# Performance work log

Measured on AMD Instinct MI355X. Metric: run time of the kernel, lower is better.

The kernel has to match this reference:

```python
import jax, jax.numpy as jnp
import numpy as np

B, Nv, Ne, Dv, De, Du = 8, 4096, 32768, 128, 128, 128
Dep, Dvp, Dup = 128, 128, 128


def setup_inputs() -> dict:
    key = jax.random.key(0)
    ks = jax.random.split(key, 11)
    s = 0.02
    return {
        "nodes": jax.random.normal(ks[0], (B, Nv, Dv), jnp.float32),
        "edges": jax.random.normal(ks[1], (B, Ne, De), jnp.float32),
        "global_u": jax.random.normal(ks[2], (B, Du), jnp.float32),
        "edge_rs": jax.random.randint(ks[3], (B, Ne, 2), 0, Nv, jnp.int32),
        "edge_masks": jax.random.randint(ks[4], (B, Ne, 1), 0, 2, jnp.int32),
        "W_edge": jax.random.normal(ks[5], (De + 2 * Dv + Du, Dep), jnp.float32) * s,
        "b_edge": jnp.zeros((Dep,), jnp.float32),
        "W_node": jax.random.normal(ks[6], (Dep + Dv + Du, Dvp), jnp.float32) * s,
        "b_node": jnp.zeros((Dvp,), jnp.float32),
        "W_glob": jax.random.normal(ks[7], (Dep + Dvp + Du, Dup), jnp.float32) * s,
        "b_glob": jnp.zeros((Dup,), jnp.float32),
    }


def reference(nodes, edges, global_u, edge_rs, edge_masks,
              W_edge, b_edge, W_node, b_node, W_glob, b_glob):
    recv = edge_rs[..., 0]  # (B,Ne)
    send = edge_rs[..., 1]
    # gather receiver / sender node features: (B,Ne,Dv)
    r_nodes = jnp.take_along_axis(nodes, jnp.broadcast_to(recv[..., None], (B, Ne, Dv)), axis=1)
    s_nodes = jnp.take_along_axis(nodes, jnp.broadcast_to(send[..., None], (B, Ne, Dv)), axis=1)
    u_e = jnp.broadcast_to(global_u[:, None, :], (B, Ne, Du))

    # edge block: MLP on concat -> (B,Ne,Dep)
    edge_in = jnp.concatenate([edges, r_nodes, s_nodes, u_e], -1)
    edges_p = jax.nn.relu(edge_in @ W_edge + b_edge)

    # e2v merge: masked segment-sum of edges onto receiver nodes -> (B,Nv,Dep)
    mask = edge_masks.astype(edges_p.dtype)  # (B,Ne,1)
    e2v = jax.vmap(lambda e, r: jax.ops.segment_sum(e, r, num_segments=Nv))(edges_p * mask, recv)

    # node block
    u_n = jnp.broadcast_to(global_u[:, None, :], (B, Nv, Du))
    node_in = jnp.concatenate([e2v, nodes, u_n], -1)
    nodes_p = jax.nn.relu(node_in @ W_node + b_node)

    # global block: sum-pool edges and nodes
    e2u = edges_p.sum(axis=1)  # (B,Dep)
    v2u = nodes_p.sum(axis=1)  # (B,Dvp)
    global_in = jnp.concatenate([e2u, v2u, global_u], -1)
    global_u_p = jax.nn.relu(global_in @ W_glob + b_glob)

    return (nodes_p, edges_p, global_u_p)
```

## Files before the change

kernel.cpp:

```cpp
#include <hip/hip_runtime.h>
#include <hip/hip_bf16.h>

#define B  8
#define NV 4096
#define NE 32768
#define D  128
#define KE2 384
#define KN2 256
#define KG 384

using short8 = __attribute__((ext_vector_type(8))) short;
using f32x4  = __attribute__((ext_vector_type(4))) float;

__device__ inline unsigned short f2bf(float f) {
    unsigned u = __builtin_bit_cast(unsigned, f);
    u += 0x7FFFu + ((u >> 16) & 1u);
    return (unsigned short)(u >> 16);
}

__device__ inline short8 cvt8(float4 a, float4 b) {
    union { __hip_bfloat162 h[4]; short8 v; } u;
    u.h[0] = __float22bfloat162_rn(make_float2(a.x, a.y));
    u.h[1] = __float22bfloat162_rn(make_float2(a.z, a.w));
    u.h[2] = __float22bfloat162_rn(make_float2(b.x, b.y));
    u.h[3] = __float22bfloat162_rn(make_float2(b.z, b.w));
    return u.v;
}

__global__ __launch_bounds__(256) void prep_weights(
    const float* __restrict__ We, const float* __restrict__ Wn,
    unsigned short* __restrict__ WtE, unsigned short* __restrict__ WtN)
{
    const int idx = blockIdx.x * 256 + threadIdx.x;
    {
        const int n = idx / KE2, k = idx % KE2;
        WtE[idx] = f2bf(We[(size_t)k * D + n]);
    }
    if (idx < 128 * KN2) {
        const int n = idx >> 8, k = idx & 255;
        WtN[idx] = f2bf(Wn[(size_t)k * D + n]);
    }
}

__global__ __launch_bounds__(128) void bias_kernel(
    const float* __restrict__ gu,
    const float* __restrict__ We, const float* __restrict__ be,
    const float* __restrict__ Wn, const float* __restrict__ bn,
    float* __restrict__ bias_e, float* __restrict__ bias_n)
{
    const int b = blockIdx.x, n = threadIdx.x;
    float se = be[n], sn = bn[n];
    for (int k = 0; k < D; ++k) {
        const float uk = gu[(size_t)b * D + k];
        se += uk * We[(size_t)(KE2 + k) * D + n];
        sn += uk * Wn[(size_t)(KN2 + k) * D + n];
    }
    bias_e[(size_t)b * D + n] = se;
    bias_n[(size_t)b * D + n] = sn;
}

__global__ __launch_bounds__(256) void hist_kernel(
    const int* __restrict__ edge_rs, const int* __restrict__ edge_masks,
    int* __restrict__ cnt)
{
    const int idx = blockIdx.x * 256 + threadIdx.x;
    if (edge_masks[idx]) {
        const int b = idx >> 15;
        const int r = edge_rs[2 * idx];
        atomicAdd(cnt + b * NV + r, 1);
    }
}

__global__ __launch_bounds__(1024) void scan_kernel(
    const int* __restrict__ cnt, int* __restrict__ off, int* __restrict__ cur)
{
    const int b = blockIdx.x, t = threadIdx.x;
    __shared__ int part[1024];
    int4 c = *(const int4*)(cnt + b * NV + t * 4);
    const int s0 = c.x, s1 = s0 + c.y, s2 = s1 + c.z, s3 = s2 + c.w;
    part[t] = s3;
    __syncthreads();
    #pragma unroll
    for (int d = 1; d < 1024; d <<= 1) {
        const int v = (t >= d) ? part[t - d] : 0;
        __syncthreads();
        part[t] += v;
        __syncthreads();
    }
    const int base = part[t] - s3;
    int* o = off + b * (NV + 1) + t * 4;
    o[0] = base; o[1] = base + s0; o[2] = base + s1; o[3] = base + s2;
    int4 cc = { base, base + s0, base + s1, base + s2 };
    *(int4*)(cur + b * NV + t * 4) = cc;
    if (t == 1023) off[b * (NV + 1) + NV] = part[1023];
}

__global__ __launch_bounds__(256) void scatter_kernel(
    const int* __restrict__ edge_rs, const int* __restrict__ edge_masks,
    int* __restrict__ cur, int* __restrict__ elist)
{
    const int idx = blockIdx.x * 256 + threadIdx.x;
    if (edge_masks[idx]) {
        const int b = idx >> 15;
        const int e = idx & (NE - 1);
        const int r = edge_rs[2 * idx];
        const int pos = atomicAdd(cur + b * NV + r, 1);
        elist[b * NE + pos] = e;
    }
}

__global__ __launch_bounds__(512, 4) void edge_kernel(
    const float* __restrict__ nodes,
    const float* __restrict__ edges,
    const int*   __restrict__ edge_rs,
    const unsigned short* __restrict__ WtE,
    const float* __restrict__ bias_e,
    float* __restrict__ edges_p,
    float* __restrict__ pe)
{
    __shared__ unsigned short Albuf[2][128 * 64];

    const int tid = threadIdx.x;
    const int b   = blockIdx.y;
    const int e0  = blockIdx.x * 128;

    const int srow = tid >> 2;
    const int sq   = tid & 3;
    const int sX   = (srow & 7) << 3;

    const int2 rs = ((const int2*)edge_rs)[(size_t)b * NE + e0 + srow];
    const float* aseg0 = edges + ((size_t)b * NE + e0 + srow) * D;
    const float* aseg1 = nodes + ((size_t)b * NV + rs.x) * D;
    const float* aseg2 = nodes + ((size_t)b * NV + rs.y) * D;

    const int lane = tid & 63;
    const int wv   = tid >> 6;
    const int wr   = wv >> 2, wc = wv & 3;
    const int lc   = lane & 15, lg = lane >> 4;
    const int lX   = (lc & 7) << 3;

    float4 av[2], av2[2];

    auto loadA = [&](int t) {
        const float* seg = (t < 2) ? aseg0 : (t < 4) ? aseg1 : aseg2;
        const float* src = seg + (t & 1) * 64 + sq * 16;
        av[0]  = *(const float4*)(src);
        av[1]  = *(const float4*)(src + 4);
        av2[0] = *(const float4*)(src + 8);
        av2[1] = *(const float4*)(src + 12);
    };
    auto writeStage = [&](int buf) {
        unsigned short* Al = Albuf[buf];
        const int g0 = sq * 16;
        *(short8*)(Al + srow * 64 + ((g0    ) ^ sX)) = cvt8(av[0], av[1]);
        *(short8*)(Al + srow * 64 + ((g0 + 8) ^ sX)) = cvt8(av2[0], av2[1]);
    };

    f32x4 acc[4][2] = {};
    auto compute = [&](int buf, int t) {
        const unsigned short* Al = Albuf[buf];
        #pragma unroll
        for (int ksub = 0; ksub < 2; ++ksub) {
            const int k = ksub * 32 + lg * 8;
            short8 afr[4], bfr[2];
            #pragma unroll
            for (int nt = 0; nt < 2; ++nt)
                bfr[nt] = *(const short8*)(WtE + (size_t)(wc * 32 + nt * 16 + lc) * KE2
                                               + t * 64 + k);
            #pragma unroll
            for (int mt = 0; mt < 4; ++mt)
                afr[mt] = *(const short8*)(Al + (wr * 64 + mt * 16 + lc) * 64 + (k ^ lX));
            #pragma unroll
            for (int mt = 0; mt < 4; ++mt)
                #pragma unroll
                for (int nt = 0; nt < 2; ++nt)
                    acc[mt][nt] = __builtin_amdgcn_mfma_f32_16x16x32_bf16(
                                      afr[mt], bfr[nt], acc[mt][nt], 0, 0, 0);
        }
    };

    loadA(0); writeStage(0);
    __syncthreads();
    #pragma unroll
    for (int t = 0; t < 6; ++t) {
        if (t < 5) loadA(t + 1);
        compute(t & 1, t);
        if (t < 5) writeStage((t + 1) & 1);
        __syncthreads();
    }

    #pragma unroll
    for (int nt = 0; nt < 2; ++nt) {
        const int col = wc * 32 + nt * 16 + lc;
        const float bias = bias_e[(size_t)b * D + col];
        float csum = 0.f;
        #pragma unroll
        for (int mt = 0; mt < 4; ++mt)
            #pragma unroll
            for (int r = 0; r < 4; ++r) {
                const int row = wr * 64 + mt * 16 + lg * 4 + r;
                const float v = fmaxf(acc[mt][nt][r] + bias, 0.f);
                edges_p[((size_t)b * NE + e0 + row) * D + col] = v;
                csum += v;
            }
        csum += __shfl_xor(csum, 16);
        csum += __shfl_xor(csum, 32);
        if (lg == 0)
            pe[(((size_t)b * 256 + blockIdx.x) * 2 + wr) * D + col] = csum;
    }
}

__global__ __launch_bounds__(256, 3) void node_kernel(
    const float* __restrict__ nodes,
    const float* __restrict__ edges_p,
    const int*   __restrict__ off,
    const int*   __restrict__ elist,
    const unsigned short* __restrict__ WtN,
    const float* __restrict__ bias_n,
    float* __restrict__ nodes_p,
    float* __restrict__ pn)
{
    __shared__ unsigned short Albuf[2][64 * 64];
    __shared__ unsigned short Wlbuf[2][128 * 64];

    const int tid = threadIdx.x;
    const int b   = blockIdx.y;
    const int n0  = blockIdx.x * 64;

    const int srowA = tid >> 2;
    const int sqA   = tid & 3;
    const int sXA   = (srowA & 7) << 3;
    const int srowW = tid >> 1;
    const int sqW   = tid & 1;
    const int sXW   = (srowW & 7) << 3;

    const int vtx = n0 + srowA;
    const int p0  = off[b * (NV + 1) + vtx];
    const int p1  = off[b * (NV + 1) + vtx + 1];
    const float* nsrc = nodes + ((size_t)b * NV + vtx) * D;

    const int lane = tid & 63;
    const int wv   = tid >> 6;
    const int wr   = wv >> 1, wc = wv & 1;
    const int lc   = lane & 15, lg = lane >> 4;
    const int lX   = (lc & 7) << 3;

    float4 av[2], av2[2];
    short8 wstg[4];

    auto loadA = [&](int t) {
        if (t < 2) {
            float4 s0 = {}, s1 = {}, s2 = {}, s3 = {};
            const int koff = (t & 1) * 64 + sqA * 16;
            for (int p = p0; p < p1; ++p) {
                const int e = elist[b * NE + p];
                const float* src = edges_p + ((size_t)b * NE + e) * D + koff;
                const float4 x0 = *(const float4*)(src);
                const float4 x1 = *(const float4*)(src + 4);
                const float4 x2 = *(const float4*)(src + 8);
                const float4 x3 = *(const float4*)(src + 12);
                s0.x += x0.x; s0.y += x0.y; s0.z += x0.z; s0.w += x0.w;
                s1.x += x1.x; s1.y += x1.y; s1.z += x1.z; s1.w += x1.w;
                s2.x += x2.x; s2.y += x2.y; s2.z += x2.z; s2.w += x2.w;
                s3.x += x3.x; s3.y += x3.y; s3.z += x3.z; s3.w += x3.w;
            }
            av[0] = s0; av[1] = s1; av2[0] = s2; av2[1] = s3;
        } else {
            const float* src = nsrc + (t - 2) * 64 + sqA * 16;
            av[0]  = *(const float4*)(src);
            av[1]  = *(const float4*)(src + 4);
            av2[0] = *(const float4*)(src + 8);
            av2[1] = *(const float4*)(src + 12);
        }
    };
    auto loadW = [&](int t) {
        const unsigned short* src = WtN + (size_t)srowW * KN2 + t * 64 + sqW * 32;
        wstg[0] = *(const short8*)(src);
        wstg[1] = *(const short8*)(src + 8);
        wstg[2] = *(const short8*)(src + 16);
        wstg[3] = *(const short8*)(src + 24);
    };
    auto writeStage = [&](int buf) {
        unsigned short* Al = Albuf[buf];
        const int gA = sqA * 16;
        *(short8*)(Al + srowA * 64 + ((gA    ) ^ sXA)) = cvt8(av[0], av[1]);
        *(short8*)(Al + srowA * 64 + ((gA + 8) ^ sXA)) = cvt8(av2[0], av2[1]);
        unsigned short* Wl = Wlbuf[buf];
        const int gW = sqW * 32;
        *(short8*)(Wl + srowW * 64 + ((gW     ) ^ sXW)) = wstg[0];
        *(short8*)(Wl + srowW * 64 + ((gW + 8 ) ^ sXW)) = wstg[1];
        *(short8*)(Wl + srowW * 64 + ((gW + 16) ^ sXW)) = wstg[2];
        *(short8*)(Wl + srowW * 64 + ((gW + 24) ^ sXW)) = wstg[3];
    };

    f32x4 acc[2][4] = {};
    auto compute = [&](int buf) {
        const unsigned short* Al = Albuf[buf];
        const unsigned short* Wl = Wlbuf[buf];
        #pragma unroll
        for (int ksub = 0; ksub < 2; ++ksub) {
            const int k = ksub * 32 + lg * 8;
            short8 afr[2], bfr[4];
            #pragma unroll
            for (int mt = 0; mt < 2; ++mt)
                afr[mt] = *(const short8*)(Al + (wr * 32 + mt * 16 + lc) * 64 + (k ^ lX));
            #pragma unroll
            for (int nt = 0; nt < 4; ++nt)
                bfr[nt] = *(const short8*)(Wl + (wc * 64 + nt * 16 + lc) * 64 + (k ^ lX));
            #pragma unroll
            for (int mt = 0; mt < 2; ++mt)
                #pragma unroll
                for (int nt = 0; nt < 4; ++nt)
                    acc[mt][nt] = __builtin_amdgcn_mfma_f32_16x16x32_bf16(
                                      afr[mt], bfr[nt], acc[mt][nt], 0, 0, 0);
        }
    };

    loadA(0); loadW(0); writeStage(0);
    __syncthreads();
    #pragma unroll
    for (int t = 0; t < 4; ++t) {
        if (t < 3) { loadA(t + 1); loadW(t + 1); }
        compute(t & 1);
        if (t < 3) {
            writeStage((t + 1) & 1);
            __syncthreads();
        }
    }

    #pragma unroll
    for (int nt = 0; nt < 4; ++nt) {
        const int col = wc * 64 + nt * 16 + lc;
        const float bias = bias_n[(size_t)b * D + col];
        float csum = 0.f;
        #pragma unroll
        for (int mt = 0; mt < 2; ++mt)
            #pragma unroll
            for (int r = 0; r < 4; ++r) {
                const int row = wr * 32 + mt * 16 + lg * 4 + r;
                const float v = fmaxf(acc[mt][nt][r] + bias, 0.f);
                nodes_p[((size_t)b * NV + n0 + row) * D + col] = v;
                csum += v;
            }
        csum += __shfl_xor(csum, 16);
        csum += __shfl_xor(csum, 32);
        if (lg == 0)
            pn[(((size_t)b * 64 + blockIdx.x) * 2 + wr) * D + col] = csum;
    }
}

__global__ __launch_bounds__(256) void reduce_kernel(
    const float* __restrict__ pe, const float* __restrict__ pn,
    float* __restrict__ e2u, float* __restrict__ v2u)
{
    __shared__ float redE[2][128], redN[2][128];
    const int b = blockIdx.x;
    const int j = threadIdx.x & 127;
    const int h = threadIdx.x >> 7;
    float s = 0.f;
    for (int i = h * 256; i < h * 256 + 256; ++i)
        s += pe[((size_t)b * 512 + i) * D + j];
    float t = 0.f;
    for (int i = h * 64; i < h * 64 + 64; ++i)
        t += pn[((size_t)b * 128 + i) * D + j];
    redE[h][j] = s;
    redN[h][j] = t;
    __syncthreads();
    if (h == 0) {
        e2u[(size_t)b * D + j] = redE[0][j] + redE[1][j];
        v2u[(size_t)b * D + j] = redN[0][j] + redN[1][j];
    }
}

__global__ __launch_bounds__(128) void glob_kernel(
    const float* __restrict__ e2u,
    const float* __restrict__ v2u,
    const float* __restrict__ gu,
    const float* __restrict__ W_glob,
    const float* __restrict__ b_glob,
    float* __restrict__ glob_p)
{
    __shared__ float gin[KG];
    const int b = blockIdx.x;
    const int j = threadIdx.x;

    gin[j      ] = e2u[(size_t)b * D + j];
    gin[j + 128] = v2u[(size_t)b * D + j];
    gin[j + 256] = gu [(size_t)b * D + j];
    __syncthreads();

    float acc = b_glob[j];
    #pragma unroll 4
    for (int k = 0; k < KG; ++k)
        acc += gin[k] * W_glob[(size_t)k * D + j];
    glob_p[(size_t)b * D + j] = fmaxf(acc, 0.f);
}

extern "C" void kernel_launch(void* const* d_in, const int* in_sizes, int n_in,
                              void* d_out, int out_size, void* d_ws, size_t ws_size,
                              hipStream_t stream) {
    const float* nodes      = (const float*)d_in[0];
    const float* edges      = (const float*)d_in[1];
    const float* gu         = (const float*)d_in[2];
    const int*   edge_rs    = (const int*)d_in[3];
    const int*   edge_masks = (const int*)d_in[4];
    const float* W_edge     = (const float*)d_in[5];
    const float* b_edge     = (const float*)d_in[6];
    const float* W_node     = (const float*)d_in[7];
    const float* b_node     = (const float*)d_in[8];
    const float* W_glob     = (const float*)d_in[9];
    const float* b_glob     = (const float*)d_in[10];

    float* out     = (float*)d_out;
    float* nodes_p = out;
    float* edges_p = out + (size_t)B * NV * D;
    float* glob_p  = edges_p + (size_t)B * NE * D;

    int*   cnt    = (int*)d_ws;
    int*   off    = cnt + (size_t)B * NV;
    int*   cur    = off + (size_t)B * (NV + 1);
    int*   elist  = cur + (size_t)B * NV;
    float* e2u    = (float*)(elist + (size_t)B * NE);
    float* v2u    = e2u + (size_t)B * D;
    float* bias_e = v2u + (size_t)B * D;
    float* bias_n = bias_e + (size_t)B * D;
    float* pe     = bias_n + (size_t)B * D;
    float* pn     = pe + (size_t)B * 512 * D;
    unsigned short* WtE = (unsigned short*)(pn + (size_t)B * 128 * D);
    unsigned short* WtN = WtE + 128 * KE2;

    hipMemsetAsync(cnt, 0, (size_t)B * NV * sizeof(int), stream);

    prep_weights<<<(128 * KE2) / 256, 256, 0, stream>>>(W_edge, W_node, WtE, WtN);
    bias_kernel<<<B, 128, 0, stream>>>(gu, W_edge, b_edge, W_node, b_node, bias_e, bias_n);
    hist_kernel<<<(B * NE) / 256, 256, 0, stream>>>(edge_rs, edge_masks, cnt);
    scan_kernel<<<B, 1024, 0, stream>>>(cnt, off, cur);
    scatter_kernel<<<(B * NE) / 256, 256, 0, stream>>>(edge_rs, edge_masks, cur, elist);

    dim3 eg(NE / 128, B);
    edge_kernel<<<eg, 512, 0, stream>>>(nodes, edges, edge_rs,
                                        WtE, bias_e, edges_p, pe);
    dim3 ng(NV / 64, B);
    node_kernel<<<ng, 256, 0, stream>>>(nodes, edges_p, off, elist,
                                        WtN, bias_n, nodes_p, pn);
    reduce_kernel<<<B, 256, 0, stream>>>(pe, pn, e2u, v2u);
    glob_kernel<<<B, 128, 0, stream>>>(e2u, v2u, gu, W_glob, b_glob, glob_p);
}
```

Before: 211.0 us.

## Precompute per-node projections before gathering so edge GEMM shrinks to K=128

Splits the edge MLP algebraically. The receiver and sender node features are multiplied by their weight slices once per node in a new gemm_nodes_kernel, and the results are stored in bf16 in Yp. The edge kernel then runs only the edges·W1 GEMM and gathers the precomputed projections for each edge's endpoints. The node kernel likewise reads its nodes·W projection from Yp. This cuts the edge GEMM's K from 384 to 128 and replaces per-edge gathers of fp32 node rows with bf16 projection rows, at the cost of an extra kernel, more workspace and an added bf16 rounding of intermediates. The grids are also flattened with the batch index innermost, and the double-buffered K loop is dropped in favour of a single full 128-wide LDS tile.

After: 205.5 us. -2.6%, faster.

```diff
diff --git a/kernel.cpp b/kernel.cpp
--- a/kernel.cpp
+++ b/kernel.cpp
@@ -17,7 +17,10 @@
     u += 0x7FFFu + ((u >> 16) & 1u);
     return (unsigned short)(u >> 16);
 }
-
+__device__ inline float bf2f(unsigned short h) {
+    unsigned u = ((unsigned)h) << 16;
+    return __builtin_bit_cast(float, u);
+}
 __device__ inline short8 cvt8(float4 a, float4 b) {
     union { __hip_bfloat162 h[4]; short8 v; } u;
     u.h[0] = __float22bfloat162_rn(make_float2(a.x, a.y));
@@ -29,17 +32,18 @@
 
 __global__ __launch_bounds__(256) void prep_weights(
     const float* __restrict__ We, const float* __restrict__ Wn,
-    unsigned short* __restrict__ WtE, unsigned short* __restrict__ WtN)
-{
-    const int idx = blockIdx.x * 256 + threadIdx.x;
-    {
-        const int n = idx / KE2, k = idx % KE2;
-        WtE[idx] = f2bf(We[(size_t)k * D + n]);
-    }
-    if (idx < 128 * KN2) {
-        const int n = idx >> 8, k = idx & 255;
-        WtN[idx] = f2bf(Wn[(size_t)k * D + n]);
-    }
+    unsigned short* __restrict__ WtE1, unsigned short* __restrict__ WtP,
+    unsigned short* __restrict__ WtN1)
+{
+    const int idx   = blockIdx.x * 256 + threadIdx.x;
+    const int which = idx >> 14;
+    const int r     = idx & 16383;
+    const int n     = r >> 7, k = r & 127;
+    if (which == 0)      WtE1[r]             = f2bf(We[(size_t)k * D + n]);
+    else if (which == 1) WtP[r]              = f2bf(We[(size_t)(128 + k) * D + n]);
+    else if (which == 2) WtP[16384 + r]      = f2bf(We[(size_t)(256 + k) * D + n]);
+    else if (which == 3) WtP[2 * 16384 + r]  = f2bf(Wn[(size_t)(128 + k) * D + n]);
+    else                 WtN1[r]             = f2bf(Wn[(size_t)k * D + n]);
 }
 
 __global__ __launch_bounds__(128) void bias_kernel(
@@ -109,89 +113,165 @@
     }
 }
 
-__global__ __launch_bounds__(512, 4) void edge_kernel(
+__global__ __launch_bounds__(512, 4) void gemm_nodes_kernel(
     const float* __restrict__ nodes,
-    const float* __restrict__ edges,
-    const int*   __restrict__ edge_rs,
-    const unsigned short* __restrict__ WtE,
-    const float* __restrict__ bias_e,
-    float* __restrict__ edges_p,
-    float* __restrict__ pe)
-{
-    __shared__ unsigned short Albuf[2][128 * 64];
-
-    const int tid = threadIdx.x;
-    const int b   = blockIdx.y;
-    const int e0  = blockIdx.x * 128;
+    const unsigned short* __restrict__ WtP,
+    unsigned short* __restrict__ Yp)
+{
+    __shared__ unsigned short Ash[128 * 128];
+    __shared__ unsigned short Wsh[128 * 128];
+
+    const int tid  = threadIdx.x;
+    const int bid  = blockIdx.x;
+    const int b    = bid & 7;
+    const int rest = bid >> 3;
+    const int tile = rest & 31;
+    const int part = rest >> 5;
+    const int n0   = tile * 128;
 
     const int srow = tid >> 2;
     const int sq   = tid & 3;
     const int sX   = (srow & 7) << 3;
 
-    const int2 rs = ((const int2*)edge_rs)[(size_t)b * NE + e0 + srow];
-    const float* aseg0 = edges + ((size_t)b * NE + e0 + srow) * D;
-    const float* aseg1 = nodes + ((size_t)b * NV + rs.x) * D;
-    const float* aseg2 = nodes + ((size_t)b * NV + rs.y) * D;
+    {
+        const float* src = nodes + ((size_t)b * NV + n0 + srow) * D + sq * 32;
+        #pragma unroll
+        for (int j = 0; j < 4; ++j) {
+            const float4 a = *(const float4*)(src + j * 8);
+            const float4 c = *(const float4*)(src + j * 8 + 4);
+            *(short8*)(Ash + srow * 128 + ((sq * 32 + j * 8) ^ sX)) = cvt8(a, c);
+        }
+        const unsigned short* ws = WtP + (size_t)part * 16384 + srow * 128 + sq * 32;
+        #pragma unroll
+        for (int j = 0; j < 4; ++j)
+            *(short8*)(Wsh + srow * 128 + ((sq * 32 + j * 8) ^ sX)) = *(const short8*)(ws + j * 8);
+    }
+    __syncthreads();
 
     const int lane = tid & 63;
     const int wv   = tid >> 6;
     const int wr   = wv >> 2, wc = wv & 3;
     const int lc   = lane & 15, lg = lane >> 4;
-    const int lX   = (lc & 7) << 3;
-
-    float4 av[2], av2[2];
-
-    auto loadA = [&](int t) {
-        const float* seg = (t < 2) ? aseg0 : (t < 4) ? aseg1 : aseg2;
-        const float* src = seg + (t & 1) * 64 + sq * 16;
-        av[0]  = *(const float4*)(src);
-        av[1]  = *(const float4*)(src + 4);
-        av2[0] = *(const float4*)(src + 8);
-        av2[1] = *(const float4*)(src + 12);
-    };
-    auto writeStage = [&](int buf) {
-        unsigned short* Al = Albuf[buf];
-        const int g0 = sq * 16;
-        *(short8*)(Al + srow * 64 + ((g0    ) ^ sX)) = cvt8(av[0], av[1]);
-        *(short8*)(Al + srow * 64 + ((g0 + 8) ^ sX)) = cvt8(av2[0], av2[1]);
-    };
 
     f32x4 acc[4][2] = {};
-    auto compute = [&](int buf, int t) {
-        const unsigned short* Al = Albuf[buf];
-        #pragma unroll
-        for (int ksub = 0; ksub < 2; ++ksub) {
-            const int k = ksub * 32 + lg * 8;
-            short8 afr[4], bfr[2];
+    #pragma unroll
+    for (int ksub = 0; ksub < 4; ++ksub) {
+        const int k = ksub * 32 + lg * 8;
+        short8 afr[4], bfr[2];
+        #pragma unroll
+        for (int mt = 0; mt < 4; ++mt) {
+            const int row = wr * 64 + mt * 16 + lc;
+            afr[mt] = *(const short8*)(Ash + row * 128 + (k ^ ((row & 7) << 3)));
+        }
+        #pragma unroll
+        for (int nt = 0; nt < 2; ++nt) {
+            const int row = wc * 32 + nt * 16 + lc;
+            bfr[nt] = *(const short8*)(Wsh + row * 128 + (k ^ ((row & 7) << 3)));
+        }
+        #pragma unroll
+        for (int mt = 0; mt < 4; ++mt)
             #pragma unroll
             for (int nt = 0; nt < 2; ++nt)
-                bfr[nt] = *(const short8*)(WtE + (size_t)(wc * 32 + nt * 16 + lc) * KE2
-                                               + t * 64 + k);
-            #pragma unroll
-            for (int mt = 0; mt < 4; ++mt)
-                afr[mt] = *(const short8*)(Al + (wr * 64 + mt * 16 + lc) * 64 + (k ^ lX));
-            #pragma unroll
-            for (int mt = 0; mt < 4; ++mt)
-                #pragma unroll
-                for (int nt = 0; nt < 2; ++nt)
-                    acc[mt][nt] = __builtin_amdgcn_mfma_f32_16x16x32_bf16(
-                                      afr[mt], bfr[nt], acc[mt][nt], 0, 0, 0);
-        }
-    };
-
-    loadA(0); writeStage(0);
-    __syncthreads();
-    #pragma unroll
-    for (int t = 0; t < 6; ++t) {
-        if (t < 5) loadA(t + 1);
-        compute(t & 1, t);
-        if (t < 5) writeStage((t + 1) & 1);
-        __syncthreads();
+                acc[mt][nt] = __builtin_amdgcn_mfma_f32_16x16x32_bf16(
+                                  afr[mt], bfr[nt], acc[mt][nt], 0, 0, 0);
     }
 
     #pragma unroll
     for (int nt = 0; nt < 2; ++nt) {
         const int col = wc * 32 + nt * 16 + lc;
+        #pragma unroll
+        for (int mt = 0; mt < 4; ++mt)
+            #pragma unroll
+            for (int r = 0; r < 4; ++r) {
+                const int row = wr * 64 + mt * 16 + lg * 4 + r;
+                Yp[((size_t)b * NV + n0 + row) * 384 + part * 128 + col] =
+                    f2bf(acc[mt][nt][r]);
+            }
+    }
+}
+
+__global__ __launch_bounds__(512, 4) void edge_kernel(
+    const float* __restrict__ edges,
+    const int*   __restrict__ edge_rs,
+    const unsigned short* __restrict__ WtE1,
+    const unsigned short* __restrict__ Yp,
+    const float* __restrict__ bias_e,
+    float* __restrict__ edges_p,
+    float* __restrict__ pe)
+{
+    __shared__ unsigned short Ash[128 * 128];
+    __shared__ unsigned short Wsh[128 * 128];
+
+    const int tid  = threadIdx.x;
+    const int bid  = blockIdx.x;
+    const int b    = bid & 7;
+    const int tile = bid >> 3;
+    const int e0   = tile * 128;
+
+    const int srow = tid >> 2;
+    const int sq   = tid & 3;
+    const int sX   = (srow & 7) << 3;
+
+    const int2 rs = ((const int2*)edge_rs)[(size_t)b * NE + e0 + srow];
+
+    {
+        const float* src = edges + ((size_t)b * NE + e0 + srow) * D + sq * 32;
+        #pragma unroll
+        for (int j = 0; j < 4; ++j) {
+            const float4 a = *(const float4*)(src + j * 8);
+            const float4 c = *(const float4*)(src + j * 8 + 4);
+            *(short8*)(Ash + srow * 128 + ((sq * 32 + j * 8) ^ sX)) = cvt8(a, c);
+        }
+        const unsigned short* ws = WtE1 + srow * 128 + sq * 32;
+        #pragma unroll
+        for (int j = 0; j < 4; ++j)
+            *(short8*)(Wsh + srow * 128 + ((sq * 32 + j * 8) ^ sX)) = *(const short8*)(ws + j * 8);
+    }
+    __syncthreads();
+
+    const int lane = tid & 63;
+    const int wv   = tid >> 6;
+    const int wr   = wv >> 2, wc = wv & 3;
+    const int lc   = lane & 15, lg = lane >> 4;
+
+    f32x4 acc[4][2] = {};
+    #pragma unroll
+    for (int ksub = 0; ksub < 4; ++ksub) {
+        const int k = ksub * 32 + lg * 8;
+        short8 afr[4], bfr[2];
+        #pragma unroll
+        for (int mt = 0; mt < 4; ++mt) {
+            const int row = wr * 64 + mt * 16 + lc;
+            afr[mt] = *(const short8*)(Ash + row * 128 + (k ^ ((row & 7) << 3)));
+        }
+        #pragma unroll
+        for (int nt = 0; nt < 2; ++nt) {
+            const int row = wc * 32 + nt * 16 + lc;
+            bfr[nt] = *(const short8*)(Wsh + row * 128 + (k ^ ((row & 7) << 3)));
+        }
+        #pragma unroll
+        for (int mt = 0; mt < 4; ++mt)
+            #pragma unroll
+            for (int nt = 0; nt < 2; ++nt)
+                acc[mt][nt] = __builtin_amdgcn_mfma_f32_16x16x32_bf16(
+                                  afr[mt], bfr[nt], acc[mt][nt], 0, 0, 0);
+    }
+    __syncthreads();
+
+    {
+        const unsigned short* y2 = Yp + ((size_t)b * NV + rs.x) * 384 +       sq * 32;
+        const unsigned short* y3 = Yp + ((size_t)b * NV + rs.y) * 384 + 128 + sq * 32;
+        #pragma unroll
+        for (int j = 0; j < 4; ++j) {
+            *(short8*)(Ash + srow * 128 + ((sq * 32 + j * 8) ^ sX)) = *(const short8*)(y2 + j * 8);
+            *(short8*)(Wsh + srow * 128 + ((sq * 32 + j * 8) ^ sX)) = *(const short8*)(y3 + j * 8);
+        }
+    }
+    __syncthreads();
+
+    #pragma unroll
+    for (int nt = 0; nt < 2; ++nt) {
+        const int col  = wc * 32 + nt * 16 + lc;
         const float bias = bias_e[(size_t)b * D + col];
         float csum = 0.f;
         #pragma unroll
@@ -199,138 +279,103 @@
             #pragma unroll
             for (int r = 0; r < 4; ++r) {
                 const int row = wr * 64 + mt * 16 + lg * 4 + r;
-                const float v = fmaxf(acc[mt][nt][r] + bias, 0.f);
+                const int sc  = col ^ ((row & 7) << 3);
+                const float y2 = bf2f(Ash[row * 128 + sc]);
+                const float y3 = bf2f(Wsh[row * 128 + sc]);
+                const float v = fmaxf(acc[mt][nt][r] + y2 + y3 + bias, 0.f);
                 edges_p[((size_t)b * NE + e0 + row) * D + col] = v;
                 csum += v;
             }
         csum += __shfl_xor(csum, 16);
         csum += __shfl_xor(csum, 32);
         if (lg == 0)
-            pe[(((size_t)b * 256 + blockIdx.x) * 2 + wr) * D + col] = csum;
+            pe[(((size_t)b * 256 + tile) * 2 + wr) * D + col] = csum;
     }
 }
 
 __global__ __launch_bounds__(256, 3) void node_kernel(
-    const float* __restrict__ nodes,
     const float* __restrict__ edges_p,
     const int*   __restrict__ off,
     const int*   __restrict__ elist,
-    const unsigned short* __restrict__ WtN,
+    const unsigned short* __restrict__ WtN1,
+    const unsigned short* __restrict__ Yp,
     const float* __restrict__ bias_n,
     float* __restrict__ nodes_p,
     float* __restrict__ pn)
 {
-    __shared__ unsigned short Albuf[2][64 * 64];
-    __shared__ unsigned short Wlbuf[2][128 * 64];
-
-    const int tid = threadIdx.x;
-    const int b   = blockIdx.y;
-    const int n0  = blockIdx.x * 64;
-
-    const int srowA = tid >> 2;
-    const int sqA   = tid & 3;
-    const int sXA   = (srowA & 7) << 3;
-    const int srowW = tid >> 1;
-    const int sqW   = tid & 1;
-    const int sXW   = (srowW & 7) << 3;
-
-    const int vtx = n0 + srowA;
-    const int p0  = off[b * (NV + 1) + vtx];
-    const int p1  = off[b * (NV + 1) + vtx + 1];
-    const float* nsrc = nodes + ((size_t)b * NV + vtx) * D;
+    __shared__ unsigned short Ash[64 * 128];
+    __shared__ unsigned short Wsh[128 * 128];
+
+    const int tid  = threadIdx.x;
+    const int bid  = blockIdx.x;
+    const int b    = bid & 7;
+    const int tile = bid >> 3;
+    const int n0   = tile * 64;
+
+    const int srow = tid >> 2;
+    const int sq   = tid & 3;
+    const int sX   = (srow & 7) << 3;
+    const int srw  = tid >> 1;
+    const int sh   = tid & 1;
+    const int sXW  = (srw & 7) << 3;
+
+    {
+        const int vtx = n0 + srow;
+        const int p0  = off[b * (NV + 1) + vtx];
+        const int p1  = off[b * (NV + 1) + vtx + 1];
+        float4 s[8] = {};
+        for (int p = p0; p < p1; ++p) {
+            const int e = elist[b * NE + p];
+            const float* src = edges_p + ((size_t)b * NE + e) * D + sq * 32;
+            #pragma unroll
+            for (int j = 0; j < 8; ++j) {
+                const float4 x = *(const float4*)(src + j * 4);
+                s[j].x += x.x; s[j].y += x.y; s[j].z += x.z; s[j].w += x.w;
+            }
+        }
+        #pragma unroll
+        for (int j = 0; j < 4; ++j)
+            *(short8*)(Ash + srow * 128 + ((sq * 32 + j * 8) ^ sX)) =
+                cvt8(s[2 * j], s[2 * j + 1]);
+
+        const unsigned short* ws = WtN1 + srw * 128 + sh * 64;
+        #pragma unroll
+        for (int j = 0; j < 8; ++j)
+            *(short8*)(Wsh + srw * 128 + ((sh * 64 + j * 8) ^ sXW)) = *(const short8*)(ws + j * 8);
+    }
+    __syncthreads();
 
     const int lane = tid & 63;
     const int wv   = tid >> 6;
     const int wr   = wv >> 1, wc = wv & 1;
     const int lc   = lane & 15, lg = lane >> 4;
-    const int lX   = (lc & 7) << 3;
-
-    float4 av[2], av2[2];
-    short8 wstg[4];
-
-    auto loadA = [&](int t) {
-        if (t < 2) {
-            float4 s0 = {}, s1 = {}, s2 = {}, s3 = {};
-            const int koff = (t & 1) * 64 + sqA * 16;
-            for (int p = p0; p < p1; ++p) {
-                const int e = elist[b * NE + p];
-                const float* src = edges_p + ((size_t)b * NE + e) * D + koff;
-                const float4 x0 = *(const float4*)(src);
-                const float4 x1 = *(const float4*)(src + 4);
-                const float4 x2 = *(const float4*)(src + 8);
-                const float4 x3 = *(const float4*)(src + 12);
-                s0.x += x0.x; s0.y += x0.y; s0.z += x0.z; s0.w += x0.w;
-                s1.x += x1.x; s1.y += x1.y; s1.z += x1.z; s1.w += x1.w;
-                s2.x += x2.x; s2.y += x2.y; s2.z += x2.z; s2.w += x2.w;
-                s3.x += x3.x; s3.y += x3.y; s3.z += x3.z; s3.w += x3.w;
-            }
-            av[0] = s0; av[1] = s1; av2[0] = s2; av2[1] = s3;
-        } else {
-            const float* src = nsrc + (t - 2) * 64 + sqA * 16;
-            av[0]  = *(const float4*)(src);
-            av[1]  = *(const float4*)(src + 4);
-            av2[0] = *(const float4*)(src + 8);
-            av2[1] = *(const float4*)(src + 12);
-        }
-    };
-    auto loadW = [&](int t) {
-        const unsigned short* src = WtN + (size_t)srowW * KN2 + t * 64 + sqW * 32;
-        wstg[0] = *(const short8*)(src);
-        wstg[1] = *(const short8*)(src + 8);
-        wstg[2] = *(const short8*)(src + 16);
-        wstg[3] = *(const short8*)(src + 24);
-    };
-    auto writeStage = [&](int buf) {
-        unsigned short* Al = Albuf[buf];
-        const int gA = sqA * 16;
-        *(short8*)(Al + srowA * 64 + ((gA    ) ^ sXA)) = cvt8(av[0], av[1]);
-        *(short8*)(Al + srowA * 64 + ((gA + 8) ^ sXA)) = cvt8(av2[0], av2[1]);
-        unsigned short* Wl = Wlbuf[buf];
-        const int gW = sqW * 32;
-        *(short8*)(Wl + srowW * 64 + ((gW     ) ^ sXW)) = wstg[0];
-        *(short8*)(Wl + srowW * 64 + ((gW + 8 ) ^ sXW)) = wstg[1];
-        *(short8*)(Wl + srowW * 64 + ((gW + 16) ^ sXW)) = wstg[2];
-        *(short8*)(Wl + srowW * 64 + ((gW + 24) ^ sXW)) = wstg[3];
-    };
 
     f32x4 acc[2][4] = {};
-    auto compute = [&](int buf) {
-        const unsigned short* Al = Albuf[buf];
-        const unsigned short* Wl = Wlbuf[buf];
-        #pragma unroll
-        for (int ksub = 0; ksub < 2; ++ksub) {
-            const int k = ksub * 32 + lg * 8;
-            short8 afr[2], bfr[4];
-            #pragma unroll
-            for (int mt = 0; mt < 2; ++mt)
-                afr[mt] = *(const short8*)(Al + (wr * 32 + mt * 16 + lc) * 64 + (k ^ lX));
+    #pragma unroll
+    for (int ksub = 0; ksub < 4; ++ksub) {
+        const int k = ksub * 32 + lg * 8;
+        short8 afr[2], bfr[4];
+        #pragma unroll
+        for (int mt = 0; mt < 2; ++mt) {
+            const int row = wr * 32 + mt * 16 + lc;
+            afr[mt] = *(const short8*)(Ash + row * 128 + (k ^ ((row & 7) << 3)));
+        }
+        #pragma unroll
+        for (int nt = 0; nt < 4; ++nt) {
+            const int row = wc * 64 + nt * 16 + lc;
+            bfr[nt] = *(const short8*)(Wsh + row * 128 + (k ^ ((row & 7) << 3)));
+        }
+        #pragma unroll
+        for (int mt = 0; mt < 2; ++mt)
             #pragma unroll
             for (int nt = 0; nt < 4; ++nt)
-                bfr[nt] = *(const short8*)(Wl + (wc * 64 + nt * 16 + lc) * 64 + (k ^ lX));
-            #pragma unroll
-            for (int mt = 0; mt < 2; ++mt)
-                #pragma unroll
-                for (int nt = 0; nt < 4; ++nt)
-                    acc[mt][nt] = __builtin_amdgcn_mfma_f32_16x16x32_bf16(
-                                      afr[mt], bfr[nt], acc[mt][nt], 0, 0, 0);
-        }
-    };
-
-    loadA(0); loadW(0); writeStage(0);
-    __syncthreads();
-    #pragma unroll
-    for (int t = 0; t < 4; ++t) {
-        if (t < 3) { loadA(t + 1); loadW(t + 1); }
-        compute(t & 1);
-        if (t < 3) {
-            writeStage((t + 1) & 1);
-            __syncthreads();
-        }
+                acc[mt][nt] = __builtin_amdgcn_mfma_f32_16x16x32_bf16(
+                                  afr[mt], bfr[nt], acc[mt][nt], 0, 0, 0);
     }
 
     #pragma unroll
     for (int nt = 0; nt < 4; ++nt) {
-        const int col = wc * 64 + nt * 16 + lc;
+        const int col  = wc * 64 + nt * 16 + lc;
         const float bias = bias_n[(size_t)b * D + col];
         float csum = 0.f;
         #pragma unroll
@@ -338,14 +383,16 @@
             #pragma unroll
             for (int r = 0; r < 4; ++r) {
                 const int row = wr * 32 + mt * 16 + lg * 4 + r;
-                const float v = fmaxf(acc[mt][nt][r] + bias, 0.f);
-                nodes_p[((size_t)b * NV + n0 + row) * D + col] = v;
-                csum += v;
+                const int v   = n0 + row;
+                const float y4 = bf2f(Yp[((size_t)b * NV + v) * 384 + 256 + col]);
+                const float val = fmaxf(acc[mt][nt][r] + y4 + bias, 0.f);
+                nodes_p[((size_t)b * NV + v) * D + col] = val;
+                csum += val;
             }
         csum += __shfl_xor(csum, 16);
         csum += __shfl_xor(csum, 32);
         if (lg == 0)
-            pn[(((size_t)b * 64 + blockIdx.x) * 2 + wr) * D + col] = csum;
+            pn[(((size_t)b * 64 + tile) * 2 + wr) * D + col] = csum;
     }
 }
 
@@ -426,23 +473,24 @@
     float* bias_n = bias_e + (size_t)B * D;
     float* pe     = bias_n + (size_t)B * D;
     float* pn     = pe + (size_t)B * 512 * D;
-    unsigned short* WtE = (unsigned short*)(pn + (size_t)B * 128 * D);
-    unsigned short* WtN = WtE + 128 * KE2;
+    unsigned short* Yp   = (unsigned short*)(pn + (size_t)B * 128 * D);
+    unsigned short* WtE1 = Yp + (size_t)B * NV * 384;
+    unsigned short* WtP  = WtE1 + 16384;
+    unsigned short* WtN1 = WtP + 3 * 16384;
 
     hipMemsetAsync(cnt, 0, (size_t)B * NV * sizeof(int), stream);
 
-    prep_weights<<<(128 * KE2) / 256, 256, 0, stream>>>(W_edge, W_node, WtE, WtN);
+    prep_weights<<<(5 * 16384) / 256, 256, 0, stream>>>(W_edge, W_node, WtE1, WtP, WtN1);
     bias_kernel<<<B, 128, 0, stream>>>(gu, W_edge, b_edge, W_node, b_node, bias_e, bias_n);
     hist_kernel<<<(B * NE) / 256, 256, 0, stream>>>(edge_rs, edge_masks, cnt);
     scan_kernel<<<B, 1024, 0, stream>>>(cnt, off, cur);
     scatter_kernel<<<(B * NE) / 256, 256, 0, stream>>>(edge_rs, edge_masks, cur, elist);
 
-    dim3 eg(NE / 128, B);
-    edge_kernel<<<eg, 512, 0, stream>>>(nodes, edges, edge_rs,
-                                        WtE, bias_e, edges_p, pe);
-    dim3 ng(NV / 64, B);
-    node_kernel<<<ng, 256, 0, stream>>>(nodes, edges_p, off, elist,
-                                        WtN, bias_n, nodes_p, pn);
+    gemm_nodes_kernel<<<3 * 32 * B, 512, 0, stream>>>(nodes, WtP, Yp);
+    edge_kernel<<<(NE / 128) * B, 512, 0, stream>>>(edges, edge_rs, WtE1, Yp,
+                                                    bias_e, edges_p, pe);
+    node_kernel<<<(NV / 64) * B, 256, 0, stream>>>(edges_p, off, elist, WtN1, Yp,
+                                                   bias_n, nodes_p, pn);
     reduce_kernel<<<B, 256, 0, stream>>>(pe, pn, e2u, v2u);
     glob_kernel<<<B, 128, 0, stream>>>(e2u, v2u, gu, W_glob, b_glob, glob_p);
 }
```
